# Optimization experiments

Measured on AMD Instinct MI355X. Metric: run time of the kernel, lower is better.

## Reference

```python
import jax, jax.numpy as jnp
import numpy as np

B_SZ, T, IN_DIM, N_STATES, OUT_DIM = 64, 1024, 256, 512, 256


def setup_inputs() -> dict:
    key = jax.random.key(0)
    ks = jax.random.split(key, 5)
    def g(k, shp, sc):
        return jax.random.normal(k, shp, dtype=jnp.float32) * sc
    return {
        "x": g(ks[0], (B_SZ, T, IN_DIM), 1.0),
        "A": g(ks[1], (N_STATES, N_STATES), 1.0 / np.sqrt(N_STATES)),
        "Bm": g(ks[2], (IN_DIM, N_STATES), 1.0 / np.sqrt(IN_DIM)),
        "b": jnp.zeros((N_STATES,), jnp.float32),
        "C": g(ks[3], (N_STATES, OUT_DIM), 1.0 / np.sqrt(N_STATES)),
        "c": jnp.zeros((OUT_DIM,), jnp.float32),
        "D": g(ks[4], (N_STATES, OUT_DIM), 1.0 / np.sqrt(N_STATES)),
        "d": jnp.zeros((OUT_DIM,), jnp.float32),
    }


def reference(x, A, Bm, b, C, c, D, d):
    # x: [B, T, IN] -> time-major [T, B, IN] (mirrors tf.transpose perm=[1,0,2])
    xT = jnp.transpose(x, (1, 0, 2))
    s0 = jnp.zeros((x.shape[0], A.shape[0]), x.dtype)  # get_init_state: zeros [B, num_states]

    def step(state, xt):
        # nonlinear SSM cell: state update + Gaussian output params
        new_state = jnp.tanh(xt @ Bm + state @ A + b)
        loc = new_state @ C + c
        scale = jax.nn.softplus(new_state @ D + d)  # scale_diag > 0
        # emit stacked [2, B, OUT] (loc, scale) and the PRE-update state
        return new_state, (jnp.stack([loc, scale], axis=0), state)

    _, (ys, prev_states) = jax.lax.scan(step, s0, xT)
    # ys: [T, 2, B, OUT] -> [2, B, T, OUT] (tf perm [1,2,0,3])
    outputs = jnp.transpose(ys, (1, 2, 0, 3))
    state_out = prev_states[-1]  # state before the last cell update
    return outputs, state_out
```

## Files before the change

kernel.cpp:

```cpp
#include <hip/hip_runtime.h>
#include <hip/hip_bf16.h>
#include <cstdint>


typedef _Float16 f16;
typedef _Float16 f16x2 __attribute__((ext_vector_type(2)));
typedef _Float16 f16x4 __attribute__((ext_vector_type(4)));
typedef _Float16 f16x8 __attribute__((ext_vector_type(8)));
typedef float    f32x4 __attribute__((ext_vector_type(4)));

#define NS 512

#define OFF_S16   (0ull)
#define OFF_X16   (0ull)
#define OFF_U16   (67108864ull)
#define OFF_BMT   (134217728ull)
#define OFF_CDT   (134479872ull)
#define OFF_APREP (135004160ull)
#define OFF_ALDS  (135200768ull)
#define OFF_ASTR  (135299072ull)

#if defined(__has_builtin)
#  if __has_builtin(__builtin_amdgcn_fdot2)
#    define HAS_FDOT2 1
#  endif
#endif

__device__ __forceinline__ float fdot2f(unsigned a, unsigned s, float c) {
#ifdef HAS_FDOT2
  return __builtin_amdgcn_fdot2(__builtin_bit_cast(f16x2, a),
                                __builtin_bit_cast(f16x2, s), c, false);
#else
  f16x2 av = __builtin_bit_cast(f16x2, a);
  f16x2 sv = __builtin_bit_cast(f16x2, s);
  return c + (float)av[0] * (float)sv[0] + (float)av[1] * (float)sv[1];
#endif
}

__device__ __forceinline__ unsigned packh2(float a, float b) {
  f16x2 h; h[0] = (f16)a; h[1] = (f16)b;
  return __builtin_bit_cast(unsigned, h);
}


__global__ void ck_x(const float* __restrict__ xg, f16* __restrict__ x16) {
  int i = (blockIdx.x * 256 + threadIdx.x) * 4;
  float4 v = *(const float4*)(xg + i);
  f16x4 h; h[0] = (f16)v.x; h[1] = (f16)v.y; h[2] = (f16)v.z; h[3] = (f16)v.w;
  *(f16x4*)(x16 + i) = h;
}

__global__ void ck_bmt(const float* __restrict__ Bm, f16* __restrict__ BmT) {
  int g = blockIdx.x * 256 + threadIdx.x;
  int n = g >> 8, k = g & 255;
  BmT[g] = (f16)Bm[k * 512 + n];
}

__global__ void ck_cdt(const float* __restrict__ C, const float* __restrict__ D,
                       f16* __restrict__ CDT) {
  int g = blockIdx.x * 256 + threadIdx.x;
  int n = g >> 9, k = g & 511;
  float v = (n < 256) ? C[k * 256 + n] : D[k * 256 + (n - 256)];
  CDT[g] = (f16)v;
}

__global__ void ck_a(const float* __restrict__ Ag, unsigned* __restrict__ Aprep,
                     unsigned* __restrict__ Alds, unsigned* __restrict__ Astr) {
  int g = blockIdx.x * 256 + threadIdx.x;
  if (g < 24576) {
    int F = g >> 2, d = g & 3;
    int t = F & 511, q = F >> 9;
    int pl = q >> 1, jj2 = q & 1;
    int kb = t >> 6, l = t & 63;
    int jj = jj2 * 4 + d;
    int k0 = kb * 64 + 2 * pl;
    int j = jj * 64 + l;
    Alds[g] = packh2(Ag[k0 * 512 + j], Ag[(k0 + 1) * 512 + j]);
  } else if (g < 73728) {
    int h = g - 24576;
    int t = h / 96, rr = h % 96;
    int P = rr >> 3, jj = rr & 7;
    int kb = t >> 6, l = t & 63;
    int k0 = kb * 64 + 12 + 2 * P;
    int j = jj * 64 + l;
    Aprep[h] = packh2(Ag[k0 * 512 + j], Ag[(k0 + 1) * 512 + j]);
  } else {
    int q2 = g - 73728;
    int F = q2 >> 2, d = q2 & 3;
    int t = F & 511, f = F >> 9;
    int pp = f >> 1, jj2 = f & 1;
    int kb = t >> 6, l = t & 63;
    int jj = jj2 * 4 + d;
    int k0 = kb * 64 + 36 + 2 * pp;
    int j = jj * 64 + l;
    Astr[q2] = packh2(Ag[k0 * 512 + j], Ag[(k0 + 1) * 512 + j]);
  }
}

template <int KDIM, int MODE>
__global__ __launch_bounds__(256, 2) void gemm_kernel(
    const f16* __restrict__ Ag, const f16* __restrict__ Bt,
    const float* __restrict__ bias0, const float* __restrict__ bias1,
    void* __restrict__ outp) {
  __shared__ f16 At[128 * 40];
  __shared__ f16 Bs[128 * 40];
  const int tid = threadIdx.x;
  const int m0 = blockIdx.y * 128;
  const int n0 = blockIdx.x * 128;
  const int w = tid >> 6, lane = tid & 63;
  const int wm = w & 1, wn = w >> 1;
  const int r = lane & 15, qd = lane >> 4;

  f32x4 zero4 = {0.f, 0.f, 0.f, 0.f};
  f32x4 acc[4][4];
#pragma unroll
  for (int mt = 0; mt < 4; ++mt)
#pragma unroll
    for (int nt = 0; nt < 4; ++nt) acc[mt][nt] = zero4;

  for (int kk = 0; kk < KDIM; kk += 32) {
#pragma unroll
    for (int s = 0; s < 2; ++s) {
      int fi = tid * 2 + s;
      int row = fi >> 2, q = fi & 3;
      float4 av = *(const float4*)(Ag + (size_t)(m0 + row) * KDIM + kk + q * 8);
      *(float4*)(At + row * 40 + q * 8) = av;
      float4 bv = *(const float4*)(Bt + (size_t)(n0 + row) * KDIM + kk + q * 8);
      *(float4*)(Bs + row * 40 + q * 8) = bv;
    }
    __syncthreads();
    f16x8 af[4], bf[4];
#pragma unroll
    for (int mt = 0; mt < 4; ++mt)
      af[mt] = *(const f16x8*)(At + (wm * 64 + mt * 16 + r) * 40 + qd * 8);
#pragma unroll
    for (int nt = 0; nt < 4; ++nt)
      bf[nt] = *(const f16x8*)(Bs + (wn * 64 + nt * 16 + r) * 40 + qd * 8);
#pragma unroll
    for (int mt = 0; mt < 4; ++mt)
#pragma unroll
      for (int nt = 0; nt < 4; ++nt)
        acc[mt][nt] = __builtin_amdgcn_mfma_f32_16x16x32_f16(af[mt], bf[nt],
                                                             acc[mt][nt], 0, 0, 0);
    __syncthreads();
  }

#pragma unroll
  for (int mt = 0; mt < 4; ++mt) {
#pragma unroll
    for (int nt = 0; nt < 4; ++nt) {
      int n = n0 + wn * 64 + nt * 16 + r;
#pragma unroll
      for (int i = 0; i < 4; ++i) {
        int m = m0 + wm * 64 + mt * 16 + qd * 4 + i;
        float v = acc[mt][nt][i];
        if (MODE == 0) {
          ((f16*)outp)[(size_t)m * NS + n] = (f16)(v + bias0[n]);
        } else {
          if (n < 256) {
            ((float*)outp)[(size_t)m * 256 + n] = v + bias0[n];
          } else {
            float z = v + bias1[n - 256];
            float sp = (z > 20.f) ? z : log1pf(__expf(z));
            ((float*)outp)[16777216ull + (size_t)m * 256 + (n - 256)] = sp;
          }
        }
      }
    }
  }
}


#define BCU(x) __builtin_bit_cast(unsigned, (x))

#define REGDOT(P, SC)                                   \
  do {                                                  \
    unsigned sb_ = BCU(SC);                             \
    float4 a0_ = areg[(P) * 2], a1_ = areg[(P) * 2 + 1];\
    acc0 = fdot2f(BCU(a0_.x), sb_, acc0);               \
    acc1 = fdot2f(BCU(a0_.y), sb_, acc1);               \
    acc2 = fdot2f(BCU(a0_.z), sb_, acc2);               \
    acc3 = fdot2f(BCU(a0_.w), sb_, acc3);               \
    acc4 = fdot2f(BCU(a1_.x), sb_, acc4);               \
    acc5 = fdot2f(BCU(a1_.y), sb_, acc5);               \
    acc6 = fdot2f(BCU(a1_.z), sb_, acc6);               \
    acc7 = fdot2f(BCU(a1_.w), sb_, acc7);               \
  } while (0)

#define GAPDOT(LO, HI, SC)                              \
  do {                                                  \
    unsigned sb_ = BCU(SC);                             \
    acc0 = fdot2f(BCU((LO).x), sb_, acc0);              \
    acc1 = fdot2f(BCU((LO).y), sb_, acc1);              \
    acc2 = fdot2f(BCU((LO).z), sb_, acc2);              \
    acc3 = fdot2f(BCU((LO).w), sb_, acc3);              \
    acc4 = fdot2f(BCU((HI).x), sb_, acc4);              \
    acc5 = fdot2f(BCU((HI).y), sb_, acc5);              \
    acc6 = fdot2f(BCU((HI).z), sb_, acc6);              \
    acc7 = fdot2f(BCU((HI).w), sb_, acc7);              \
  } while (0)

__global__ __launch_bounds__(512, 2) void scan_kernel(
    const float4* __restrict__ Aprep4, const float4* __restrict__ Alds4,
    const float4* __restrict__ Astr4, const f16* __restrict__ U16,
    f16* __restrict__ S16, float* __restrict__ stout) {
  __shared__ __align__(16) f16 ldsA[49152];
  __shared__ float part[4096];
  __shared__ __align__(16) f16 sh[512];
  const int t = threadIdx.x;
  const int b = blockIdx.x;
  const int kb = t >> 6;
  const int l = t & 63;

  float4* ldsA4 = (float4*)ldsA;
#pragma unroll
  for (int q = 0; q < 12; ++q) ldsA4[q * 512 + t] = Alds4[q * 512 + t];

  float4 areg[24];
#pragma unroll
  for (int i = 0; i < 24; ++i) areg[i] = Aprep4[t * 24 + i];

  sh[t] = (f16)0.f;
  __syncthreads();

  const float4* sp4 = (const float4*)sh;
  float ns_prev = 0.f;

#pragma unroll 1
  for (int ts = 0; ts < 1024; ++ts) {
    int zoff;
    asm volatile("s_mov_b32 %0, 0" : "=s"(zoff));
    const float4* astr = Astr4 + zoff + t;

    const int row = b * 1024 + ts;
    if (ts) S16[(size_t)(row - 1) * 512 + t] = (f16)ns_prev;
    f16 uh = U16[(size_t)row * 512 + t];

    float4 g0 = astr[0 * 512], g1 = astr[1 * 512];
    float4 g2 = astr[2 * 512], g3 = astr[3 * 512];
    float4 g4 = astr[4 * 512], g5 = astr[5 * 512];
    float4 g6 = astr[6 * 512], g7 = astr[7 * 512];

    float acc0 = 0.f, acc1 = 0.f, acc2 = 0.f, acc3 = 0.f;
    float acc4 = 0.f, acc5 = 0.f, acc6 = 0.f, acc7 = 0.f;

    {
      float4 s4 = sp4[kb * 8 + 0];
      float4 L0 = ldsA4[0 * 512 + t], L1 = ldsA4[1 * 512 + t];
      float4 L2 = ldsA4[2 * 512 + t], L3 = ldsA4[3 * 512 + t];
      float4 L4 = ldsA4[4 * 512 + t], L5 = ldsA4[5 * 512 + t];
      float4 L6 = ldsA4[6 * 512 + t], L7 = ldsA4[7 * 512 + t];
      GAPDOT(L0, L1, s4.x);
      GAPDOT(L2, L3, s4.y);
      GAPDOT(L4, L5, s4.z);
      GAPDOT(L6, L7, s4.w);
    }
    {
      float4 s4 = sp4[kb * 8 + 1];
      float4 L8 = ldsA4[8 * 512 + t],  L9  = ldsA4[9 * 512 + t];
      float4 L10 = ldsA4[10 * 512 + t], L11 = ldsA4[11 * 512 + t];
      GAPDOT(L8, L9, s4.x);
      GAPDOT(L10, L11, s4.y);
      REGDOT(0, s4.z);
      REGDOT(1, s4.w);
    }

    float4 h0 = astr[8 * 512],  h1 = astr[9 * 512];
    float4 h2 = astr[10 * 512], h3 = astr[11 * 512];
    float4 h4 = astr[12 * 512], h5 = astr[13 * 512];
    float4 h6 = astr[14 * 512], h7 = astr[15 * 512];

    {
      float4 s4 = sp4[kb * 8 + 2];
      REGDOT(2, s4.x); REGDOT(3, s4.y); REGDOT(4, s4.z); REGDOT(5, s4.w);
    }
    {
      float4 s4 = sp4[kb * 8 + 3];
      REGDOT(6, s4.x); REGDOT(7, s4.y); REGDOT(8, s4.z); REGDOT(9, s4.w);
    }
    {
      float4 s4 = sp4[kb * 8 + 4];
      REGDOT(10, s4.x); REGDOT(11, s4.y);
      GAPDOT(g0, g1, s4.z);
      GAPDOT(g2, g3, s4.w);
    }
    {
      float4 s4 = sp4[kb * 8 + 5];
      GAPDOT(g4, g5, s4.x);
      GAPDOT(g6, g7, s4.y);
      g0 = astr[16 * 512]; g1 = astr[17 * 512];
      g2 = astr[18 * 512]; g3 = astr[19 * 512];
      g4 = astr[20 * 512]; g5 = astr[21 * 512];
      g6 = astr[22 * 512]; g7 = astr[23 * 512];
      GAPDOT(h0, h1, s4.z);
      GAPDOT(h2, h3, s4.w);
    }
    {
      float4 s4 = sp4[kb * 8 + 6];
      GAPDOT(h4, h5, s4.x);
      GAPDOT(h6, h7, s4.y);
      h0 = astr[24 * 512]; h1 = astr[25 * 512];
      h2 = astr[26 * 512]; h3 = astr[27 * 512];
      GAPDOT(g0, g1, s4.z);
      GAPDOT(g2, g3, s4.w);
    }
    {
      float4 s4 = sp4[kb * 8 + 7];
      GAPDOT(g4, g5, s4.x);
      GAPDOT(g6, g7, s4.y);
      GAPDOT(h0, h1, s4.z);
      GAPDOT(h2, h3, s4.w);
    }

    part[kb * 512 + 0 * 64 + l] = acc0;
    part[kb * 512 + 1 * 64 + l] = acc1;
    part[kb * 512 + 2 * 64 + l] = acc2;
    part[kb * 512 + 3 * 64 + l] = acc3;
    part[kb * 512 + 4 * 64 + l] = acc4;
    part[kb * 512 + 5 * 64 + l] = acc5;
    part[kb * 512 + 6 * 64 + l] = acc6;
    part[kb * 512 + 7 * 64 + l] = acc7;
    __syncthreads();

    float sum = (float)uh;
#pragma unroll
    for (int k2 = 0; k2 < 8; ++k2) sum += part[k2 * 512 + t];
    float e = __expf(2.f * sum);
    float ns = 1.f - 2.f / (e + 1.f);

    sh[t] = (f16)ns;
    ns_prev = ns;
    if (ts == 1022) stout[b * 512 + t] = ns;
    __syncthreads();
  }

  S16[(size_t)(b * 1024 + 1023) * 512 + t] = (f16)ns_prev;
}


extern "C" void kernel_launch(void* const* d_in, const int* in_sizes, int n_in,
                              void* d_out, int out_size, void* d_ws, size_t ws_size,
                              hipStream_t stream) {
  (void)in_sizes; (void)n_in; (void)out_size; (void)ws_size;
  const float* xg  = (const float*)d_in[0];
  const float* Ag  = (const float*)d_in[1];
  const float* Bmg = (const float*)d_in[2];
  const float* bg  = (const float*)d_in[3];
  const float* Cg  = (const float*)d_in[4];
  const float* cg  = (const float*)d_in[5];
  const float* Dg  = (const float*)d_in[6];
  const float* dg  = (const float*)d_in[7];

  char* w = (char*)d_ws;
  f16* x16 = (f16*)(w + OFF_X16);
  f16* U16 = (f16*)(w + OFF_U16);
  f16* S16 = (f16*)(w + OFF_S16);
  f16* BmT = (f16*)(w + OFF_BMT);
  f16* CDT = (f16*)(w + OFF_CDT);
  unsigned* Aprep = (unsigned*)(w + OFF_APREP);
  unsigned* Alds  = (unsigned*)(w + OFF_ALDS);
  unsigned* Astr  = (unsigned*)(w + OFF_ASTR);
  float* out = (float*)d_out;

  ck_x  <<<16384, 256, 0, stream>>>(xg, x16);
  ck_bmt<<<  512, 256, 0, stream>>>(Bmg, BmT);
  ck_cdt<<< 1024, 256, 0, stream>>>(Cg, Dg, CDT);
  ck_a  <<<  512, 256, 0, stream>>>(Ag, Aprep, Alds, Astr);

  gemm_kernel<256, 0><<<dim3(4, 512), 256, 0, stream>>>(x16, BmT, bg, nullptr,
                                                        (void*)U16);
  scan_kernel<<<64, 512, 0, stream>>>((const float4*)Aprep, (const float4*)Alds,
                                      (const float4*)Astr, U16, S16,
                                      out + 33554432);
  gemm_kernel<512, 1><<<dim3(4, 512), 256, 0, stream>>>(S16, CDT, cg, dg,
                                                        (void*)out);
}
```

Baseline: 2.549 ms.

## Stream all non-LDS A slices from global instead of holding them in registers

After: 3.819 ms. 49.8% more time.

```diff
diff --git a/kernel.cpp b/kernel.cpp
--- a/kernel.cpp
+++ b/kernel.cpp
@@ -16,9 +16,8 @@
 #define OFF_U16   (67108864ull)
 #define OFF_BMT   (134217728ull)
 #define OFF_CDT   (134479872ull)
-#define OFF_APREP (135004160ull)
-#define OFF_ALDS  (135200768ull)
-#define OFF_ASTR  (135299072ull)
+#define OFF_ALDS  (135004160ull)
+#define OFF_ASTR  (135102464ull)
 
 #if defined(__has_builtin)
 #  if __has_builtin(__builtin_amdgcn_fdot2)
@@ -64,8 +63,8 @@
   CDT[g] = (f16)v;
 }
 
-__global__ void ck_a(const float* __restrict__ Ag, unsigned* __restrict__ Aprep,
-                     unsigned* __restrict__ Alds, unsigned* __restrict__ Astr) {
+__global__ void ck_a(const float* __restrict__ Ag, unsigned* __restrict__ Alds,
+                     unsigned* __restrict__ Astr) {
   int g = blockIdx.x * 256 + threadIdx.x;
   if (g < 24576) {
     int F = g >> 2, d = g & 3;
@@ -76,24 +75,16 @@
     int k0 = kb * 64 + 2 * pl;
     int j = jj * 64 + l;
     Alds[g] = packh2(Ag[k0 * 512 + j], Ag[(k0 + 1) * 512 + j]);
-  } else if (g < 73728) {
-    int h = g - 24576;
-    int t = h / 96, rr = h % 96;
-    int P = rr >> 3, jj = rr & 7;
-    int kb = t >> 6, l = t & 63;
-    int k0 = kb * 64 + 12 + 2 * P;
-    int j = jj * 64 + l;
-    Aprep[h] = packh2(Ag[k0 * 512 + j], Ag[(k0 + 1) * 512 + j]);
   } else {
-    int q2 = g - 73728;
-    int F = q2 >> 2, d = q2 & 3;
+    int qs = g - 24576;
+    int F = qs >> 2, d = qs & 3;
     int t = F & 511, f = F >> 9;
     int pp = f >> 1, jj2 = f & 1;
     int kb = t >> 6, l = t & 63;
     int jj = jj2 * 4 + d;
-    int k0 = kb * 64 + 36 + 2 * pp;
+    int k0 = kb * 64 + 12 + 2 * pp;
     int j = jj * 64 + l;
-    Astr[q2] = packh2(Ag[k0 * 512 + j], Ag[(k0 + 1) * 512 + j]);
+    Astr[qs] = packh2(Ag[k0 * 512 + j], Ag[(k0 + 1) * 512 + j]);
   }
 }
 
@@ -173,20 +164,6 @@
 
 #define BCU(x) __builtin_bit_cast(unsigned, (x))
 
-#define REGDOT(P, SC)                                   \
-  do {                                                  \
-    unsigned sb_ = BCU(SC);                             \
-    float4 a0_ = areg[(P) * 2], a1_ = areg[(P) * 2 + 1];\
-    acc0 = fdot2f(BCU(a0_.x), sb_, acc0);               \
-    acc1 = fdot2f(BCU(a0_.y), sb_, acc1);               \
-    acc2 = fdot2f(BCU(a0_.z), sb_, acc2);               \
-    acc3 = fdot2f(BCU(a0_.w), sb_, acc3);               \
-    acc4 = fdot2f(BCU(a1_.x), sb_, acc4);               \
-    acc5 = fdot2f(BCU(a1_.y), sb_, acc5);               \
-    acc6 = fdot2f(BCU(a1_.z), sb_, acc6);               \
-    acc7 = fdot2f(BCU(a1_.w), sb_, acc7);               \
-  } while (0)
-
 #define GAPDOT(LO, HI, SC)                              \
   do {                                                  \
     unsigned sb_ = BCU(SC);                             \
@@ -201,9 +178,9 @@
   } while (0)
 
 __global__ __launch_bounds__(512, 2) void scan_kernel(
-    const float4* __restrict__ Aprep4, const float4* __restrict__ Alds4,
-    const float4* __restrict__ Astr4, const f16* __restrict__ U16,
-    f16* __restrict__ S16, float* __restrict__ stout) {
+    const float4* __restrict__ Alds4, const float4* __restrict__ Astr4,
+    const f16* __restrict__ U16, f16* __restrict__ S16,
+    float* __restrict__ stout) {
   __shared__ __align__(16) f16 ldsA[49152];
   __shared__ float part[4096];
   __shared__ __align__(16) f16 sh[512];
@@ -216,10 +193,6 @@
 #pragma unroll
   for (int q = 0; q < 12; ++q) ldsA4[q * 512 + t] = Alds4[q * 512 + t];
 
-  float4 areg[24];
-#pragma unroll
-  for (int i = 0; i < 24; ++i) areg[i] = Aprep4[t * 24 + i];
-
   sh[t] = (f16)0.f;
   __syncthreads();
 
@@ -236,10 +209,18 @@
     if (ts) S16[(size_t)(row - 1) * 512 + t] = (f16)ns_prev;
     f16 uh = U16[(size_t)row * 512 + t];
 
-    float4 g0 = astr[0 * 512], g1 = astr[1 * 512];
-    float4 g2 = astr[2 * 512], g3 = astr[3 * 512];
-    float4 g4 = astr[4 * 512], g5 = astr[5 * 512];
-    float4 g6 = astr[6 * 512], g7 = astr[7 * 512];
+    float4 x0 = astr[0 * 512],  x1 = astr[1 * 512];
+    float4 x2 = astr[2 * 512],  x3 = astr[3 * 512];
+    float4 x4 = astr[4 * 512],  x5 = astr[5 * 512];
+    float4 x6 = astr[6 * 512],  x7 = astr[7 * 512];
+    float4 y0 = astr[8 * 512],  y1 = astr[9 * 512];
+    float4 y2 = astr[10 * 512], y3 = astr[11 * 512];
+    float4 y4 = astr[12 * 512], y5 = astr[13 * 512];
+    float4 y6 = astr[14 * 512], y7 = astr[15 * 512];
+    float4 z0 = astr[16 * 512], z1 = astr[17 * 512];
+    float4 z2 = astr[18 * 512], z3 = astr[19 * 512];
+    float4 z4 = astr[20 * 512], z5 = astr[21 * 512];
+    float4 z6 = astr[22 * 512], z7 = astr[23 * 512];
 
     float acc0 = 0.f, acc1 = 0.f, acc2 = 0.f, acc3 = 0.f;
     float acc4 = 0.f, acc5 = 0.f, acc6 = 0.f, acc7 = 0.f;
@@ -257,59 +238,68 @@
     }
     {
       float4 s4 = sp4[kb * 8 + 1];
-      float4 L8 = ldsA4[8 * 512 + t],  L9  = ldsA4[9 * 512 + t];
+      float4 L8  = ldsA4[8 * 512 + t],  L9  = ldsA4[9 * 512 + t];
       float4 L10 = ldsA4[10 * 512 + t], L11 = ldsA4[11 * 512 + t];
       GAPDOT(L8, L9, s4.x);
       GAPDOT(L10, L11, s4.y);
-      REGDOT(0, s4.z);
-      REGDOT(1, s4.w);
-    }
-
-    float4 h0 = astr[8 * 512],  h1 = astr[9 * 512];
-    float4 h2 = astr[10 * 512], h3 = astr[11 * 512];
-    float4 h4 = astr[12 * 512], h5 = astr[13 * 512];
-    float4 h6 = astr[14 * 512], h7 = astr[15 * 512];
-
+      GAPDOT(x0, x1, s4.z);
+      GAPDOT(x2, x3, s4.w);
+    }
     {
       float4 s4 = sp4[kb * 8 + 2];
-      REGDOT(2, s4.x); REGDOT(3, s4.y); REGDOT(4, s4.z); REGDOT(5, s4.w);
+      GAPDOT(x4, x5, s4.x);
+      GAPDOT(x6, x7, s4.y);
+      x0 = astr[24 * 512]; x1 = astr[25 * 512];
+      x2 = astr[26 * 512]; x3 = astr[27 * 512];
+      x4 = astr[28 * 512]; x5 = astr[29 * 512];
+      x6 = astr[30 * 512]; x7 = astr[31 * 512];
+      GAPDOT(y0, y1, s4.z);
+      GAPDOT(y2, y3, s4.w);
     }
     {
       float4 s4 = sp4[kb * 8 + 3];
-      REGDOT(6, s4.x); REGDOT(7, s4.y); REGDOT(8, s4.z); REGDOT(9, s4.w);
+      GAPDOT(y4, y5, s4.x);
+      GAPDOT(y6, y7, s4.y);
+      y0 = astr[32 * 512]; y1 = astr[33 * 512];
+      y2 = astr[34 * 512]; y3 = astr[35 * 512];
+      y4 = astr[36 * 512]; y5 = astr[37 * 512];
+      y6 = astr[38 * 512]; y7 = astr[39 * 512];
+      GAPDOT(z0, z1, s4.z);
+      GAPDOT(z2, z3, s4.w);
     }
     {
       float4 s4 = sp4[kb * 8 + 4];
-      REGDOT(10, s4.x); REGDOT(11, s4.y);
-      GAPDOT(g0, g1, s4.z);
-      GAPDOT(g2, g3, s4.w);
+      GAPDOT(z4, z5, s4.x);
+      GAPDOT(z6, z7, s4.y);
+      z0 = astr[40 * 512]; z1 = astr[41 * 512];
+      z2 = astr[42 * 512]; z3 = astr[43 * 512];
+      z4 = astr[44 * 512]; z5 = astr[45 * 512];
+      z6 = astr[46 * 512]; z7 = astr[47 * 512];
+      GAPDOT(x0, x1, s4.z);
+      GAPDOT(x2, x3, s4.w);
     }
     {
       float4 s4 = sp4[kb * 8 + 5];
-      GAPDOT(g4, g5, s4.x);
-      GAPDOT(g6, g7, s4.y);
-      g0 = astr[16 * 512]; g1 = astr[17 * 512];
-      g2 = astr[18 * 512]; g3 = astr[19 * 512];
-      g4 = astr[20 * 512]; g5 = astr[21 * 512];
-      g6 = astr[22 * 512]; g7 = astr[23 * 512];
-      GAPDOT(h0, h1, s4.z);
-      GAPDOT(h2, h3, s4.w);
+      GAPDOT(x4, x5, s4.x);
+      GAPDOT(x6, x7, s4.y);
+      x0 = astr[48 * 512]; x1 = astr[49 * 512];
+      x2 = astr[50 * 512]; x3 = astr[51 * 512];
+      GAPDOT(y0, y1, s4.z);
+      GAPDOT(y2, y3, s4.w);
     }
     {
       float4 s4 = sp4[kb * 8 + 6];
-      GAPDOT(h4, h5, s4.x);
-      GAPDOT(h6, h7, s4.y);
-      h0 = astr[24 * 512]; h1 = astr[25 * 512];
-      h2 = astr[26 * 512]; h3 = astr[27 * 512];
-      GAPDOT(g0, g1, s4.z);
-      GAPDOT(g2, g3, s4.w);
+      GAPDOT(y4, y5, s4.x);
+      GAPDOT(y6, y7, s4.y);
+      GAPDOT(z0, z1, s4.z);
+      GAPDOT(z2, z3, s4.w);
     }
     {
       float4 s4 = sp4[kb * 8 + 7];
-      GAPDOT(g4, g5, s4.x);
-      GAPDOT(g6, g7, s4.y);
-      GAPDOT(h0, h1, s4.z);
-      GAPDOT(h2, h3, s4.w);
+      GAPDOT(z4, z5, s4.x);
+      GAPDOT(z6, z7, s4.y);
+      GAPDOT(x0, x1, s4.z);
+      GAPDOT(x2, x3, s4.w);
     }
 
     part[kb * 512 + 0 * 64 + l] = acc0;
@@ -357,7 +347,6 @@
   f16* S16 = (f16*)(w + OFF_S16);
   f16* BmT = (f16*)(w + OFF_BMT);
   f16* CDT = (f16*)(w + OFF_CDT);
-  unsigned* Aprep = (unsigned*)(w + OFF_APREP);
   unsigned* Alds  = (unsigned*)(w + OFF_ALDS);
   unsigned* Astr  = (unsigned*)(w + OFF_ASTR);
   float* out = (float*)d_out;
@@ -365,13 +354,12 @@
   ck_x  <<<16384, 256, 0, stream>>>(xg, x16);
   ck_bmt<<<  512, 256, 0, stream>>>(Bmg, BmT);
   ck_cdt<<< 1024, 256, 0, stream>>>(Cg, Dg, CDT);
-  ck_a  <<<  512, 256, 0, stream>>>(Ag, Aprep, Alds, Astr);
+  ck_a  <<<  512, 256, 0, stream>>>(Ag, Alds, Astr);
 
   gemm_kernel<256, 0><<<dim3(4, 512), 256, 0, stream>>>(x16, BmT, bg, nullptr,
                                                         (void*)U16);
-  scan_kernel<<<64, 512, 0, stream>>>((const float4*)Aprep, (const float4*)Alds,
-                                      (const float4*)Astr, U16, S16,
-                                      out + 33554432);
+  scan_kernel<<<64, 512, 0, stream>>>((const float4*)Alds, (const float4*)Astr,
+                                      U16, S16, out + 33554432);
   gemm_kernel<512, 1><<<dim3(4, 512), 256, 0, stream>>>(S16, CDT, cg, dg,
                                                         (void*)out);
 }
```
